# Kernel tuning notes

Measured on AMD Instinct MI355X. Metric: run time of the kernel, lower is better.

## Reference

```python
import jax, jax.numpy as jnp
import numpy as np

BETA = 0.25


def setup_inputs() -> dict:
    key = jax.random.key(0)
    k1, k2 = jax.random.split(key)
    x = jax.random.normal(k1, (32768, 512), dtype=jnp.float32)
    centroids = jax.random.normal(k2, (8192, 512), dtype=jnp.float32)
    return {"x": x, "centroids": centroids}


def reference(x, centroids):
    # x: [N, D], centroids: [K, D]
    x_norm = jnp.sum(x * x, axis=1, keepdims=True)          # [N, 1]
    c_norm = jnp.sum(centroids * centroids, axis=1)         # [K]
    xy = jnp.einsum('nd,kd->nk', x, centroids)              # [N, K]
    distances = x_norm + c_norm[None, :] - 2.0 * xy         # [N, K]
    indices = jnp.argmin(distances, axis=-1)                # [N]
    q = centroids[indices]                                  # [N, D] gather
    # losses: commitment = mse(sg(q), x); codebook = mse(q, sg(x))
    sg = jax.lax.stop_gradient
    commitment_loss = jnp.mean((sg(q) - x) ** 2)
    codebook_loss = jnp.mean((q - sg(x)) ** 2)
    loss = codebook_loss + BETA * commitment_loss
    # straight-through estimator
    x_q = x + sg(q - x)
    return (x_q, loss, indices)
```

## Files before the change

### kernel.cpp

```cpp
#include <hip/hip_runtime.h>
#include <hip/hip_bf16.h>

#define N_ROWS 32768
#define DIM    512
#define K_CENT 8192

#define LOSS_OFF 16777216u
#define IDX_OFF  16777217u

#define XH_OFF_B   0u
#define CH_OFF_B   33554432u
#define CN_OFF_B   41943040u
#define CAND_OFF_B 41975808u

#define CAND_BYTES 4194304u
#define CN_BYTES   32768u

#define BM 128
#define BN 128
#define KQ 2048
#define NKT (KQ / BN)
#define NQ  (K_CENT / KQ)

typedef __bf16 bf16x8 __attribute__((ext_vector_type(8)));
typedef float  f32x4  __attribute__((ext_vector_type(4)));

__device__ __forceinline__ unsigned short f2bf(float f) {
    unsigned u = __float_as_uint(f);
    return (unsigned short)((u + 0x7fffu + ((u >> 16) & 1u)) >> 16);
}

__device__ __forceinline__ void glds16(void* lds, const void* g) {
    __builtin_amdgcn_global_load_lds(
        (const __attribute__((address_space(1))) unsigned*)g,
        (__attribute__((address_space(3))) unsigned*)lds, 16, 0, 0);
}

__device__ __forceinline__ void ce(float& da, int& ia, float& db, int& ib) {
    bool sw = (db < da) || (db == da && ib < ia);
    float td = sw ? db : da; int ti = sw ? ib : ia;
    float ud = sw ? da : db; int ui = sw ? ia : ib;
    da = td; ia = ti; db = ud; ib = ui;
}
__device__ __forceinline__ void lmin(float da, int ia, float db, int ib,
                                     float& od, int& oi) {
    bool sw = (db < da) || (db == da && ib < ia);
    od = sw ? db : da; oi = sw ? ib : ia;
}

__global__ void __launch_bounds__(256) convert_kernel(const float* __restrict__ x,
                                                      const float* __restrict__ c,
                                                      unsigned short* __restrict__ xh,
                                                      unsigned short* __restrict__ ch,
                                                      float* __restrict__ cnp) {
    const int wave = threadIdx.x >> 6, lane = threadIdx.x & 63;
    const int gid = blockIdx.x * 4 + wave;
    if (gid < N_ROWS) {
        const float* p = x + (size_t)gid * DIM + lane * 8;
        float4 a = *(const float4*)p, b = *(const float4*)(p + 4);
        uint4 w;
        w.x = (unsigned)f2bf(a.x) | ((unsigned)f2bf(a.y) << 16);
        w.y = (unsigned)f2bf(a.z) | ((unsigned)f2bf(a.w) << 16);
        w.z = (unsigned)f2bf(b.x) | ((unsigned)f2bf(b.y) << 16);
        w.w = (unsigned)f2bf(b.z) | ((unsigned)f2bf(b.w) << 16);
        *(uint4*)(xh + (size_t)gid * DIM + lane * 8) = w;
    } else {
        const int cr = gid - N_ROWS;
        const float* p = c + (size_t)cr * DIM + lane * 8;
        float4 a = *(const float4*)p, b = *(const float4*)(p + 4);
        uint4 w;
        w.x = (unsigned)f2bf(a.x) | ((unsigned)f2bf(a.y) << 16);
        w.y = (unsigned)f2bf(a.z) | ((unsigned)f2bf(a.w) << 16);
        w.z = (unsigned)f2bf(b.x) | ((unsigned)f2bf(b.y) << 16);
        w.w = (unsigned)f2bf(b.z) | ((unsigned)f2bf(b.w) << 16);
        *(uint4*)(ch + (size_t)cr * DIM + lane * 8) = w;
        float s = a.x*a.x + a.y*a.y + a.z*a.z + a.w*a.w
                + b.x*b.x + b.y*b.y + b.z*b.z + b.w*b.w;
#pragma unroll
        for (int off = 32; off; off >>= 1) s += __shfl_down(s, off, 64);
        if (lane == 0) cnp[cr] = s;
    }
}

__global__ void __launch_bounds__(256, 2) vq_main(const unsigned short* __restrict__ xh,
                                                  const unsigned short* __restrict__ ch,
                                                  const float* __restrict__ cnp,
                                                  float* __restrict__ cand) {
    __shared__ __align__(16) unsigned short xs[BM * 32];
    __shared__ __align__(16) unsigned short cs[BN * 32];
    __shared__ float sh_d[2][BM][4];
    __shared__ int   sh_i[2][BM][4];

    const int tid  = threadIdx.x;
    const int wave = tid >> 6, lane = tid & 63;
    const int wm   = wave >> 1, wk = wave & 1;
    const int lr   = lane & 15, quad = lane >> 4;
    const int nbase = blockIdx.x * BM;
    const int h     = blockIdx.y;
    const int kc0   = h * KQ;

    const int srow = wave * 32 + (lane >> 2);
    const int scol = (lane & 3) * 8;
    const unsigned short* xg0 = xh + (size_t)(nbase + srow) * DIM + scol;
    unsigned short* xd0 = &xs[wave * 1024];
    unsigned short* xd1 = &xs[wave * 1024 + 512];
    unsigned short* cd0 = &cs[wave * 1024];
    unsigned short* cd1 = &cs[wave * 1024 + 512];

    int aoff[4], boff[4];
#pragma unroll
    for (int t = 0; t < 4; ++t) {
        aoff[t] = (wm * 64 + t * 16 + lr) * 32 + quad * 8;
        boff[t] = (wk * 64 + t * 16 + lr) * 32 + quad * 8;
    }

    float rd1[4][4], rd2[4][4];
    int   ri1[4][4], ri2[4][4];
#pragma unroll
    for (int mt = 0; mt < 4; ++mt)
#pragma unroll
        for (int r = 0; r < 4; ++r) {
            rd1[mt][r] = 1e30f; rd2[mt][r] = 1e30f;
            ri1[mt][r] = 0x7ffffff0; ri2[mt][r] = 0x7ffffff1;
        }

    for (int kt = 0; kt < NKT; ++kt) {
        const int kc = kc0 + kt * BN;
        const unsigned short* cg0 = ch + (size_t)(kc + srow) * DIM + scol;
        f32x4 acc[4][4];
#pragma unroll
        for (int mt = 0; mt < 4; ++mt)
#pragma unroll
            for (int t = 0; t < 4; ++t) { acc[mt][t].x = 0.f; acc[mt][t].y = 0.f; acc[mt][t].z = 0.f; acc[mt][t].w = 0.f; }

        for (int dsb = 0; dsb < 16; ++dsb) {
            const int d0 = dsb * 32;
            __syncthreads();
            glds16(xd0, xg0 + d0);
            glds16(xd1, xg0 + (size_t)16 * DIM + d0);
            glds16(cd0, cg0 + d0);
            glds16(cd1, cg0 + (size_t)16 * DIM + d0);
            __syncthreads();

            bf16x8 bfr[4];
#pragma unroll
            for (int t = 0; t < 4; ++t) bfr[t] = *(const bf16x8*)&cs[boff[t]];
#pragma unroll
            for (int mt = 0; mt < 4; ++mt) {
                bf16x8 a = *(const bf16x8*)&xs[aoff[mt]];
#pragma unroll
                for (int t = 0; t < 4; ++t)
                    acc[mt][t] = __builtin_amdgcn_mfma_f32_16x16x32_bf16(a, bfr[t], acc[mt][t], 0, 0, 0);
            }
        }

#pragma unroll
        for (int t = 0; t < 4; ++t) {
            const int col = kc + wk * 64 + t * 16 + lr;
            const float cnv = cnp[col];
#pragma unroll
            for (int mt = 0; mt < 4; ++mt)
#pragma unroll
                for (int r = 0; r < 4; ++r) {
                    float d = fmaf(-2.f, acc[mt][t][r], cnv);
                    bool b1 = d < rd1[mt][r];
                    bool b2 = d < rd2[mt][r];
                    float o1 = rd1[mt][r]; int oi1 = ri1[mt][r];
                    rd2[mt][r] = b1 ? o1 : (b2 ? d : rd2[mt][r]);
                    ri2[mt][r] = b1 ? oi1 : (b2 ? col : ri2[mt][r]);
                    rd1[mt][r] = b1 ? d : o1;
                    ri1[mt][r] = b1 ? col : oi1;
                }
        }
    }

#pragma unroll
    for (int mt = 0; mt < 4; ++mt)
#pragma unroll
        for (int r = 0; r < 4; ++r) {
            float a0 = rd1[mt][r], a1 = rd2[mt][r], a2 = 1e30f, a3 = 1e30f;
            int   i0 = ri1[mt][r], i1 = ri2[mt][r], i2 = 0x7ffffff2, i3 = 0x7ffffff3;
#pragma unroll
            for (int s = 1; s < 16; s <<= 1) {
                float p0 = __shfl_xor(a0, s, 64), p1 = __shfl_xor(a1, s, 64);
                float p2 = __shfl_xor(a2, s, 64), p3 = __shfl_xor(a3, s, 64);
                int   q0 = __shfl_xor(i0, s, 64), q1 = __shfl_xor(i1, s, 64);
                int   q2 = __shfl_xor(i2, s, 64), q3 = __shfl_xor(i3, s, 64);
                float l0, l1, l2, l3; int m0, m1, m2, m3;
                lmin(a0, i0, p3, q3, l0, m0);
                lmin(a1, i1, p2, q2, l1, m1);
                lmin(a2, i2, p1, q1, l2, m2);
                lmin(a3, i3, p0, q0, l3, m3);
                ce(l0, m0, l2, m2); ce(l1, m1, l3, m3);
                ce(l0, m0, l1, m1); ce(l2, m2, l3, m3);
                a0 = l0; a1 = l1; a2 = l2; a3 = l3;
                i0 = m0; i1 = m1; i2 = m2; i3 = m3;
            }
            if (lr == 0) {
                const int rl = wm * 64 + mt * 16 + quad * 4 + r;
                sh_d[wk][rl][0] = a0; sh_i[wk][rl][0] = i0;
                sh_d[wk][rl][1] = a1; sh_i[wk][rl][1] = i1;
                sh_d[wk][rl][2] = a2; sh_i[wk][rl][2] = i2;
                sh_d[wk][rl][3] = a3; sh_i[wk][rl][3] = i3;
            }
        }
    __syncthreads();

    if (tid < BM) {
        float a0 = sh_d[0][tid][0], a1 = sh_d[0][tid][1];
        float a2 = sh_d[0][tid][2], a3 = sh_d[0][tid][3];
        int   i0 = sh_i[0][tid][0], i1 = sh_i[0][tid][1];
        int   i2 = sh_i[0][tid][2], i3 = sh_i[0][tid][3];
        float b0 = sh_d[1][tid][0], b1 = sh_d[1][tid][1];
        float b2 = sh_d[1][tid][2], b3 = sh_d[1][tid][3];
        int   j0 = sh_i[1][tid][0], j1 = sh_i[1][tid][1];
        int   j2 = sh_i[1][tid][2], j3 = sh_i[1][tid][3];
        float l0, l1, l2, l3; int m0, m1, m2, m3;
        lmin(a0, i0, b3, j3, l0, m0);
        lmin(a1, i1, b2, j2, l1, m1);
        lmin(a2, i2, b1, j1, l2, m2);
        lmin(a3, i3, b0, j0, l3, m3);
        ce(l0, m0, l2, m2); ce(l1, m1, l3, m3);
        ce(l0, m0, l1, m1); ce(l2, m2, l3, m3);
        float* cell = cand + ((size_t)(nbase + tid) * NQ + h) * 8;
        cell[0] = l0; cell[1] = (float)m0;
        cell[2] = l1; cell[3] = (float)m1;
        cell[4] = l2; cell[5] = (float)m2;
        cell[6] = l3; cell[7] = (float)m3;
    }
}

__global__ void __launch_bounds__(256) vq_refine(const float* __restrict__ x,
                                                 const float* __restrict__ cg,
                                                 const float* __restrict__ cand,
                                                 float* __restrict__ outp,
                                                 int write_xq) {
    __shared__ double ls[4];
    const int wave = threadIdx.x >> 6, lane = threadIdx.x & 63;
    const int n = blockIdx.x * 4 + wave;
    const float* cell = cand + (size_t)n * 32;

    const float* xr = x + (size_t)n * DIM + lane * 8;
    float4 xa = *(const float4*)xr;
    float4 xb = *(const float4*)(xr + 4);

    double bd = 1e300; int bi = 0x7fffffff;
    float4 va = xa, vb = xb;

#pragma unroll
    for (int batch = 0; batch < 2; ++batch) {
        int kid[8];
#pragma unroll
        for (int j = 0; j < 8; ++j) kid[j] = (int)cell[(batch * 8 + j) * 2 + 1];

        float4 ca[8], cb[8];
#pragma unroll
        for (int j = 0; j < 8; ++j) {
            const float* cr = cg + (size_t)kid[j] * DIM + lane * 8;
            ca[j] = *(const float4*)cr;
            cb[j] = *(const float4*)(cr + 4);
        }

#pragma unroll
        for (int j = 0; j < 8; ++j) {
            const int k = kid[j];
            double s = 0.0, t;
            t = (double)xa.x - (double)ca[j].x; s += t * t;
            t = (double)xa.y - (double)ca[j].y; s += t * t;
            t = (double)xa.z - (double)ca[j].z; s += t * t;
            t = (double)xa.w - (double)ca[j].w; s += t * t;
            t = (double)xb.x - (double)cb[j].x; s += t * t;
            t = (double)xb.y - (double)cb[j].y; s += t * t;
            t = (double)xb.z - (double)cb[j].z; s += t * t;
            t = (double)xb.w - (double)cb[j].w; s += t * t;
#pragma unroll
            for (int off = 32; off; off >>= 1) s += __shfl_down(s, off, 64);
            s = __shfl(s, 0, 64);
            bool w = (s < bd) || (s == bd && k < bi);
            bd = w ? s : bd;
            bi = w ? k : bi;
            va.x = w ? ca[j].x : va.x; va.y = w ? ca[j].y : va.y;
            va.z = w ? ca[j].z : va.z; va.w = w ? ca[j].w : va.w;
            vb.x = w ? cb[j].x : vb.x; vb.y = w ? cb[j].y : vb.y;
            vb.z = w ? cb[j].z : vb.z; vb.w = w ? cb[j].w : vb.w;
        }
    }
    if (write_xq) {
        float* row = outp + (size_t)n * DIM + lane * 8;
        *(float4*)row = va;
        *(float4*)(row + 4) = vb;
    }
    if (lane == 0) { outp[IDX_OFF + n] = (float)bi; ls[wave] = bd; }
    __syncthreads();
    if (threadIdx.x == 0)
        atomicAdd(outp + LOSS_OFF,
                  (float)((ls[0] + ls[1] + ls[2] + ls[3]) * (1.25 / 16777216.0)));
}

__global__ void __launch_bounds__(256) vq_gather(const float* __restrict__ cg,
                                                 float* __restrict__ outp) {
    const int wave = threadIdx.x >> 6, lane = threadIdx.x & 63;
    const int n = blockIdx.x * 4 + wave;
    const int k = (int)outp[IDX_OFF + n];
    const float* cr = cg + (size_t)k * DIM + lane * 8;
    float4 a = *(const float4*)cr;
    float4 b = *(const float4*)(cr + 4);
    float* row = outp + (size_t)n * DIM + lane * 8;
    *(float4*)row = a;
    *(float4*)(row + 4) = b;
}

extern "C" void kernel_launch(void* const* d_in, const int* in_sizes, int n_in,
                              void* d_out, int out_size, void* d_ws, size_t ws_size,
                              hipStream_t stream) {
    const float* x   = (const float*)d_in[0];
    const float* cen = (const float*)d_in[1];
    float* out = (float*)d_out;

    unsigned short* xh  = (unsigned short*)((char*)d_out + XH_OFF_B);
    unsigned short* chp = (unsigned short*)((char*)d_out + CH_OFF_B);

    const int fused = (d_ws != nullptr) && (ws_size >= (size_t)(CAND_BYTES + CN_BYTES));
    float* cand = fused ? (float*)d_ws
                        : (float*)((char*)d_out + CAND_OFF_B);
    float* cnp  = fused ? (float*)((char*)d_ws + CAND_BYTES)
                        : (float*)((char*)d_out + CN_OFF_B);

    hipMemsetAsync((void*)(out + LOSS_OFF), 0, sizeof(float), stream);
    convert_kernel<<<(N_ROWS + K_CENT) / 4, 256, 0, stream>>>(x, cen, xh, chp, cnp);
    dim3 g2(N_ROWS / BM, NQ);
    vq_main<<<g2, 256, 0, stream>>>(xh, chp, cnp, cand);
    vq_refine<<<N_ROWS / 4, 256, 0, stream>>>(x, cen, cand, out, fused);
    if (!fused) vq_gather<<<N_ROWS / 4, 256, 0, stream>>>(cen, out);
}
```

Baseline: 692.3 us.

## Pipeline LDS staging with 4-deep ring buffer, swizzle, and halve centroid split

Replaces the double-barrier synchronous LDS load per 32-wide D slice with a 4-stage ring buffer prefetched three slices ahead via global_load_lds, using a single barrier and vmcnt wait per step. It adds an XOR swizzle on LDS layout to reduce bank conflicts. The centroid range is split in two halves instead of four, which halves the candidate count the refine kernel must check (8 instead of 16). LDS grows to 64KB per block, which may lower occupancy, and fewer candidates slightly raises the risk of missing the true argmin.

```diff
diff --git a/kernel.cpp b/kernel.cpp
--- a/kernel.cpp
+++ b/kernel.cpp
@@ -13,14 +13,14 @@
 #define CN_OFF_B   41943040u
 #define CAND_OFF_B 41975808u
 
-#define CAND_BYTES 4194304u
+#define CAND_BYTES 2097152u
 #define CN_BYTES   32768u
 
 #define BM 128
 #define BN 128
-#define KQ 2048
-#define NKT (KQ / BN)
-#define NQ  (K_CENT / KQ)
+#define KHALF 4096
+#define NKT (KHALF / BN)
+#define NH  2
 
 typedef __bf16 bf16x8 __attribute__((ext_vector_type(8)));
 typedef float  f32x4  __attribute__((ext_vector_type(4)));
@@ -86,8 +86,8 @@
                                                   const unsigned short* __restrict__ ch,
                                                   const float* __restrict__ cnp,
                                                   float* __restrict__ cand) {
-    __shared__ __align__(16) unsigned short xs[BM * 32];
-    __shared__ __align__(16) unsigned short cs[BN * 32];
+    __shared__ __align__(16) unsigned short xs[4 * 4096];
+    __shared__ __align__(16) unsigned short cs[4 * 4096];
     __shared__ float sh_d[2][BM][4];
     __shared__ int   sh_i[2][BM][4];
 
@@ -97,21 +97,33 @@
     const int lr   = lane & 15, quad = lane >> 4;
     const int nbase = blockIdx.x * BM;
     const int h     = blockIdx.y;
-    const int kc0   = h * KQ;
-
-    const int srow = wave * 32 + (lane >> 2);
-    const int scol = (lane & 3) * 8;
-    const unsigned short* xg0 = xh + (size_t)(nbase + srow) * DIM + scol;
-    unsigned short* xd0 = &xs[wave * 1024];
-    unsigned short* xd1 = &xs[wave * 1024 + 512];
-    unsigned short* cd0 = &cs[wave * 1024];
-    unsigned short* cd1 = &cs[wave * 1024 + 512];
+    const int kc0   = h * KHALF;
+
+    const int srow16 = lane >> 2;
+    const int sswz   = (lane & 3) ^ ((lane >> 3) & 3);
+    const unsigned short* xg0 = xh + (size_t)(nbase + wave * 32 + srow16) * DIM + sswz * 8;
+    const unsigned short* xg1 = xg0 + (size_t)16 * DIM;
+    const unsigned short* cg0 = ch + (size_t)(kc0 + wave * 32 + srow16) * DIM + sswz * 8;
+
+    unsigned short* xw = xs + wave * 1024;
+    unsigned short* cw = cs + wave * 1024;
+
+#define STAGE(ring, ktn, dd) do {                                          \
+        unsigned short* xd_ = xw + (ring) * 4096;                          \
+        unsigned short* cd_ = cw + (ring) * 4096;                          \
+        const unsigned short* cgk_ = cg0 + (size_t)(ktn) * (BN * DIM) + (dd); \
+        glds16(xd_,       xg0 + (dd));                                     \
+        glds16(xd_ + 512, xg1 + (dd));                                     \
+        glds16(cd_,       cgk_);                                           \
+        glds16(cd_ + 512, cgk_ + 16 * DIM);                                \
+    } while (0)
 
     int aoff[4], boff[4];
 #pragma unroll
     for (int t = 0; t < 4; ++t) {
-        aoff[t] = (wm * 64 + t * 16 + lr) * 32 + quad * 8;
-        boff[t] = (wk * 64 + t * 16 + lr) * 32 + quad * 8;
+        const int sw = (quad ^ ((lr >> 1) & 3)) << 4;
+        aoff[t] = (wm * 64 + t * 16 + lr) * 64 + sw;
+        boff[t] = (wk * 64 + t * 16 + lr) * 64 + sw;
     }
 
     float rd1[4][4], rd2[4][4];
@@ -124,30 +136,42 @@
             ri1[mt][r] = 0x7ffffff0; ri2[mt][r] = 0x7ffffff1;
         }
 
+    STAGE(0, 0, 0);
+    STAGE(1, 0, 32);
+    STAGE(2, 0, 64);
+    asm volatile("s_waitcnt vmcnt(0)" ::: "memory");
+    __builtin_amdgcn_s_barrier();
+
     for (int kt = 0; kt < NKT; ++kt) {
         const int kc = kc0 + kt * BN;
-        const unsigned short* cg0 = ch + (size_t)(kc + srow) * DIM + scol;
+        float cnv[4];
+#pragma unroll
+        for (int t = 0; t < 4; ++t) cnv[t] = cnp[kc + wk * 64 + t * 16 + lr];
+
         f32x4 acc[4][4];
 #pragma unroll
         for (int mt = 0; mt < 4; ++mt)
 #pragma unroll
-            for (int t = 0; t < 4; ++t) { acc[mt][t].x = 0.f; acc[mt][t].y = 0.f; acc[mt][t].z = 0.f; acc[mt][t].w = 0.f; }
-
-        for (int dsb = 0; dsb < 16; ++dsb) {
-            const int d0 = dsb * 32;
-            __syncthreads();
-            glds16(xd0, xg0 + d0);
-            glds16(xd1, xg0 + (size_t)16 * DIM + d0);
-            glds16(cd0, cg0 + d0);
-            glds16(cd1, cg0 + (size_t)16 * DIM + d0);
-            __syncthreads();
-
+            for (int t = 0; t < 4; ++t)
+                acc[mt][t] = (f32x4){0.f, 0.f, 0.f, 0.f};
+
+#pragma unroll 4
+        for (int j = 0; j < 16; ++j) {
+            asm volatile("s_waitcnt vmcnt(8)" ::: "memory");
+            __builtin_amdgcn_s_barrier();
+            if (kt < NKT - 1 || j < 13) {
+                const int jn = j + 3;
+                STAGE(jn & 3, kt + (jn >> 4), (jn & 15) * 32);
+            }
+            const char* xb = (const char*)xs + (j & 3) * 8192;
+            const char* cb = (const char*)cs + (j & 3) * 8192;
             bf16x8 bfr[4];
 #pragma unroll
-            for (int t = 0; t < 4; ++t) bfr[t] = *(const bf16x8*)&cs[boff[t]];
+            for (int t = 0; t < 4; ++t)
+                bfr[t] = *(const bf16x8*)(cb + boff[t]);
 #pragma unroll
             for (int mt = 0; mt < 4; ++mt) {
-                bf16x8 a = *(const bf16x8*)&xs[aoff[mt]];
+                bf16x8 a = *(const bf16x8*)(xb + aoff[mt]);
 #pragma unroll
                 for (int t = 0; t < 4; ++t)
                     acc[mt][t] = __builtin_amdgcn_mfma_f32_16x16x32_bf16(a, bfr[t], acc[mt][t], 0, 0, 0);
@@ -157,12 +181,11 @@
 #pragma unroll
         for (int t = 0; t < 4; ++t) {
             const int col = kc + wk * 64 + t * 16 + lr;
-            const float cnv = cnp[col];
 #pragma unroll
             for (int mt = 0; mt < 4; ++mt)
 #pragma unroll
                 for (int r = 0; r < 4; ++r) {
-                    float d = fmaf(-2.f, acc[mt][t][r], cnv);
+                    float d = fmaf(-2.f, acc[mt][t][r], cnv[t]);
                     bool b1 = d < rd1[mt][r];
                     bool b2 = d < rd2[mt][r];
                     float o1 = rd1[mt][r]; int oi1 = ri1[mt][r];
@@ -173,6 +196,7 @@
                 }
         }
     }
+#undef STAGE
 
 #pragma unroll
     for (int mt = 0; mt < 4; ++mt)
@@ -222,7 +246,7 @@
         lmin(a3, i3, b0, j0, l3, m3);
         ce(l0, m0, l2, m2); ce(l1, m1, l3, m3);
         ce(l0, m0, l1, m1); ce(l2, m2, l3, m3);
-        float* cell = cand + ((size_t)(nbase + tid) * NQ + h) * 8;
+        float* cell = cand + ((size_t)(nbase + tid) * NH + h) * 8;
         cell[0] = l0; cell[1] = (float)m0;
         cell[2] = l1; cell[3] = (float)m1;
         cell[4] = l2; cell[5] = (float)m2;
@@ -238,52 +262,47 @@
     __shared__ double ls[4];
     const int wave = threadIdx.x >> 6, lane = threadIdx.x & 63;
     const int n = blockIdx.x * 4 + wave;
-    const float* cell = cand + (size_t)n * 32;
+    const float* cell = cand + (size_t)n * 16;
+    int kid[8];
+#pragma unroll
+    for (int j = 0; j < 8; ++j) kid[j] = (int)cell[2 * j + 1];
 
     const float* xr = x + (size_t)n * DIM + lane * 8;
     float4 xa = *(const float4*)xr;
     float4 xb = *(const float4*)(xr + 4);
 
+    float4 ca[8], cb[8];
+#pragma unroll
+    for (int j = 0; j < 8; ++j) {
+        const float* cr = cg + (size_t)kid[j] * DIM + lane * 8;
+        ca[j] = *(const float4*)cr;
+        cb[j] = *(const float4*)(cr + 4);
+    }
+
     double bd = 1e300; int bi = 0x7fffffff;
     float4 va = xa, vb = xb;
-
-#pragma unroll
-    for (int batch = 0; batch < 2; ++batch) {
-        int kid[8];
-#pragma unroll
-        for (int j = 0; j < 8; ++j) kid[j] = (int)cell[(batch * 8 + j) * 2 + 1];
-
-        float4 ca[8], cb[8];
-#pragma unroll
-        for (int j = 0; j < 8; ++j) {
-            const float* cr = cg + (size_t)kid[j] * DIM + lane * 8;
-            ca[j] = *(const float4*)cr;
-            cb[j] = *(const float4*)(cr + 4);
-        }
-
-#pragma unroll
-        for (int j = 0; j < 8; ++j) {
-            const int k = kid[j];
-            double s = 0.0, t;
-            t = (double)xa.x - (double)ca[j].x; s += t * t;
-            t = (double)xa.y - (double)ca[j].y; s += t * t;
-            t = (double)xa.z - (double)ca[j].z; s += t * t;
-            t = (double)xa.w - (double)ca[j].w; s += t * t;
-            t = (double)xb.x - (double)cb[j].x; s += t * t;
-            t = (double)xb.y - (double)cb[j].y; s += t * t;
-            t = (double)xb.z - (double)cb[j].z; s += t * t;
-            t = (double)xb.w - (double)cb[j].w; s += t * t;
-#pragma unroll
-            for (int off = 32; off; off >>= 1) s += __shfl_down(s, off, 64);
-            s = __shfl(s, 0, 64);
-            bool w = (s < bd) || (s == bd && k < bi);
-            bd = w ? s : bd;
-            bi = w ? k : bi;
-            va.x = w ? ca[j].x : va.x; va.y = w ? ca[j].y : va.y;
-            va.z = w ? ca[j].z : va.z; va.w = w ? ca[j].w : va.w;
-            vb.x = w ? cb[j].x : vb.x; vb.y = w ? cb[j].y : vb.y;
-            vb.z = w ? cb[j].z : vb.z; vb.w = w ? cb[j].w : vb.w;
-        }
+#pragma unroll
+    for (int j = 0; j < 8; ++j) {
+        const int k = kid[j];
+        double s = 0.0, t;
+        t = (double)xa.x - (double)ca[j].x; s += t * t;
+        t = (double)xa.y - (double)ca[j].y; s += t * t;
+        t = (double)xa.z - (double)ca[j].z; s += t * t;
+        t = (double)xa.w - (double)ca[j].w; s += t * t;
+        t = (double)xb.x - (double)cb[j].x; s += t * t;
+        t = (double)xb.y - (double)cb[j].y; s += t * t;
+        t = (double)xb.z - (double)cb[j].z; s += t * t;
+        t = (double)xb.w - (double)cb[j].w; s += t * t;
+#pragma unroll
+        for (int off = 32; off; off >>= 1) s += __shfl_down(s, off, 64);
+        s = __shfl(s, 0, 64);
+        bool w = (s < bd) || (s == bd && k < bi);
+        bd = w ? s : bd;
+        bi = w ? k : bi;
+        va.x = w ? ca[j].x : va.x; va.y = w ? ca[j].y : va.y;
+        va.z = w ? ca[j].z : va.z; va.w = w ? ca[j].w : va.w;
+        vb.x = w ? cb[j].x : vb.x; vb.y = w ? cb[j].y : vb.y;
+        vb.z = w ? cb[j].z : vb.z; vb.w = w ? cb[j].w : vb.w;
     }
     if (write_xq) {
         float* row = outp + (size_t)n * DIM + lane * 8;
@@ -328,7 +347,7 @@
 
     hipMemsetAsync((void*)(out + LOSS_OFF), 0, sizeof(float), stream);
     convert_kernel<<<(N_ROWS + K_CENT) / 4, 256, 0, stream>>>(x, cen, xh, chp, cnp);
-    dim3 g2(N_ROWS / BM, NQ);
+    dim3 g2(N_ROWS / BM, NH);
     vq_main<<<g2, 256, 0, stream>>>(xh, chp, cnp, cand);
     vq_refine<<<N_ROWS / 4, 256, 0, stream>>>(x, cen, cand, out, fused);
     if (!fused) vq_gather<<<N_ROWS / 4, 256, 0, stream>>>(cen, out);
```

Result: faster. 632.0 us (-8.7%).
